# Performance work log

Hardware: AMD Instinct MI355X
Metric: run time of the kernel (lower is better)

The kernel has to match this reference:

```python
import jax, jax.numpy as jnp
import numpy as np

N, C, H, W = 32, 64, 128, 128
P_ROLL_H, P_ROLL_W = 1, -2  # frozen values of random.randint(-2, 2) at init

def setup_inputs() -> dict:
    key = jax.random.key(0)
    k1, k2, k3 = jax.random.split(key, 3)
    x = jax.random.normal(k1, (N, C, H, W), dtype=jnp.float32)
    # Conv2d(c, c, (1,7), dilation=(1,3), padding=(0,9), bias=False); torch default kaiming-uniform-ish, use uniform
    fan_in = C * 1 * 7
    bc = 1.0 / np.sqrt(fan_in)
    W_conv = jax.random.uniform(k2, (C, C, 1, 7), minval=-bc, maxval=bc, dtype=jnp.float32)
    # p_4_w: uniform(-sqrt(3/3), sqrt(3/3)) = uniform(-1, 1), shape (3,1)
    p4w = jax.random.uniform(k3, (3, 1), minval=-1.0, maxval=1.0, dtype=jnp.float32)
    return {"x": x, "W_conv": W_conv, "p4w": p4w}

def _dilated_unfold_h(x):
    # F.unfold(x, (3,1), dilation=(2,1), padding=(2,0)) -> (n, c, 3, h, w)
    # tap k gathers row h + 2*(k-1), zero-padded
    xp = jnp.pad(x, ((0, 0), (0, 0), (2, 2), (0, 0)))
    h = x.shape[2]
    return jnp.stack([xp[:, :, 2 * k:2 * k + h, :] for k in range(3)], axis=2)

def reference(x, W_conv, p4w):
    # t_1: dilated 3-tap unfold along h -> (n, c, 3, h, w)
    t1 = _dilated_unfold_h(x)
    # t_2: circular rolls along h and w
    t2 = jnp.roll(jnp.roll(t1, P_ROLL_H, axis=3), P_ROLL_W, axis=4)
    # t_3: conv (1,7) dilation (1,3) pad (0,9), width-preserving
    t3 = jax.lax.conv_general_dilated(
        x, W_conv, window_strides=(1, 1), padding=((0, 0), (9, 9)),
        rhs_dilation=(1, 3), dimension_numbers=("NCHW", "OIHW", "NCHW"))
    # t_4: weighted reduce over the 3 taps (einsum 'abcde,cf->abfde', f=1)
    t4 = jnp.einsum("nckhw,kf->ncfhw", t2, p4w)[:, :, 0]
    # t_6 = (x + conv(x)) * t_4
    return (x + t3) * t4
```

## Files before the change

### kernel.cpp

```cpp
#include <hip/hip_runtime.h>
#include <hip/hip_bf16.h>

#define N_ 32
#define C_ 64
#define H_ 128
#define W_ 128
#define HW_ (H_ * W_)
#define CHW_ (C_ * HW_)

#define XT_STRIDE 72
#define XT_ROWS 146
#define CB_STRIDE 130
#define SMEM_BYTES (4 * 16 * CB_STRIDE * 4)

typedef __bf16 bf16x8 __attribute__((ext_vector_type(8)));
typedef float floatx4 __attribute__((ext_vector_type(4)));

__device__ inline unsigned short f2bf(float f) {
    __hip_bfloat16 h = __float2bfloat16(f);
    return *reinterpret_cast<unsigned short*>(&h);
}

__global__ void prepack_kernel(const float* __restrict__ Wc, uint4* __restrict__ Ap) {
    int idx = blockIdx.x * 256 + threadIdx.x;
    if (idx >= 14 * 4 * 64) return;
    int lane = idx & 63;
    int mt = (idx >> 6) & 3;
    int kt = idx >> 8;
    int m = mt * 16 + (lane & 15);
    int kbase = kt * 32 + (lane >> 4) * 8;
    unsigned int r[4];
    #pragma unroll
    for (int p = 0; p < 4; ++p) {
        unsigned int half[2];
        #pragma unroll
        for (int jj = 0; jj < 2; ++jj) {
            int k = kbase + 2 * p + jj;
            int t = k >> 6;
            int i = k & 63;
            half[jj] = f2bf(Wc[m * 448 + i * 7 + t]);
        }
        r[p] = half[0] | (half[1] << 16);
    }
    Ap[idx] = make_uint4(r[0], r[1], r[2], r[3]);
}

__global__ __launch_bounds__(256) void fused_mfma_kernel(
    const float* __restrict__ x, const uint4* __restrict__ Ap,
    const float* __restrict__ p4w, float* __restrict__ out)
{
    __shared__ __attribute__((aligned(16))) char smem[SMEM_BYTES];
    unsigned short* xT = (unsigned short*)smem;
    float* convbuf = (float*)smem;

    const int b = blockIdx.x;
    const int xcd = b & 7;
    const int i_ = b >> 3;
    const int n = i_ >> 4;
    const int h = xcd * 16 + (i_ & 15);

    const int tid = threadIdx.x;
    const int wave = tid >> 6;
    const int lane = tid & 63;
    const int l16 = lane & 15;
    const int quad = lane >> 4;
    const float* xn = x + (size_t)n * CHW_;

    uint4 afrag[14];
    #pragma unroll
    for (int kt = 0; kt < 14; ++kt)
        afrag[kt] = Ap[kt * 256 + wave * 64 + lane];

    unsigned int* xz = (unsigned int*)xT;
    for (int i = tid; i < 648; i += 256) {
        int d = (i < 324) ? i : (4932 + (i - 324));
        xz[d] = 0u;
    }

    const float* xrow = xn + h * W_;
    #pragma unroll
    for (int p = 0; p < 4; ++p) {
        const int c0 = wave * 8 + (p >> 1) * 32;
        const int w = (tid & 63) + (p & 1) * 64;
        const float* src = xrow + (size_t)c0 * HW_ + w;
        unsigned int pk[4];
        #pragma unroll
        for (int i = 0; i < 4; ++i) {
            float f0 = src[(size_t)(2 * i) * HW_];
            float f1 = src[(size_t)(2 * i + 1) * HW_];
            pk[i] = (unsigned int)f2bf(f0) | ((unsigned int)f2bf(f1) << 16);
        }
        *(uint4*)&xT[(w + 9) * XT_STRIDE + c0] = make_uint4(pk[0], pk[1], pk[2], pk[3]);
    }

    __syncthreads();

    floatx4 acc[8];
    #pragma unroll
    for (int nt = 0; nt < 8; ++nt) acc[nt] = (floatx4){0.f, 0.f, 0.f, 0.f};

    const int base_half = l16 * XT_STRIDE + quad * 8;
    #pragma unroll
    for (int kt = 0; kt < 14; ++kt) {
        bf16x8 av = __builtin_bit_cast(bf16x8, afrag[kt]);
        int koff = (kt >> 1) * 3 * XT_STRIDE + (kt & 1) * 32;
        #pragma unroll
        for (int nt = 0; nt < 8; ++nt) {
            int off = base_half + koff + nt * 16 * XT_STRIDE;
            uint4 d = *(const uint4*)&xT[off];
            bf16x8 bv = __builtin_bit_cast(bf16x8, d);
            acc[nt] = __builtin_amdgcn_mfma_f32_16x16x32_bf16(av, bv, acc[nt], 0, 0, 0);
        }
    }

    __syncthreads();

    float* cw = convbuf + wave * 16 * CB_STRIDE;
    #pragma unroll
    for (int nt = 0; nt < 8; ++nt) {
        #pragma unroll
        for (int r = 0; r < 4; ++r)
            cw[(quad * 4 + r) * CB_STRIDE + nt * 16 + l16] = acc[nt][r];
    }

    const float p0 = p4w[0], p1 = p4w[1], p2 = p4w[2];
    const int h1 = (h - 1 + H_) & 127;

    #pragma unroll
    for (int j = 0; j < 8; ++j) {
        int idx = j * 64 + lane;
        int o_ = idx >> 5;
        int w4 = idx & 31;
        int w = w4 * 4;
        int o = wave * 16 + o_;

        float4 cv = *(const float4*)&cw[o_ * CB_STRIDE + w];

        const float* xc = xn + o * HW_;
        float4 xv = *(const float4*)(xc + h * W_ + w);

        int wsrc = w + 2;
        float tap[3][4];
        #pragma unroll
        for (int k = 0; k < 3; ++k) {
            int hh = h1 + 2 * k - 2;
            if (hh >= 0 && hh < H_) {
                const float* rowp = xc + hh * W_;
                float2 a = *(const float2*)(rowp + wsrc);
                float2 b2 = *(const float2*)(rowp + ((wsrc + 2) & 127));
                tap[k][0] = a.x; tap[k][1] = a.y; tap[k][2] = b2.x; tap[k][3] = b2.y;
            } else {
                tap[k][0] = tap[k][1] = tap[k][2] = tap[k][3] = 0.f;
            }
        }
        float ov[4];
        float xa[4] = {xv.x, xv.y, xv.z, xv.w};
        float ca[4] = {cv.x, cv.y, cv.z, cv.w};
        #pragma unroll
        for (int e = 0; e < 4; ++e) {
            float t4 = p0 * tap[0][e] + p1 * tap[1][e] + p2 * tap[2][e];
            ov[e] = (xa[e] + ca[e]) * t4;
        }
        *(float4*)(out + (size_t)n * CHW_ + o * HW_ + h * W_ + w) =
            make_float4(ov[0], ov[1], ov[2], ov[3]);
    }
}

extern "C" void kernel_launch(void* const* d_in, const int* in_sizes, int n_in,
                              void* d_out, int out_size, void* d_ws, size_t ws_size,
                              hipStream_t stream) {
    const float* x   = (const float*)d_in[0];
    const float* Wc  = (const float*)d_in[1];
    const float* p4w = (const float*)d_in[2];
    float* out       = (float*)d_out;
    uint4* Apack     = (uint4*)d_ws;

    prepack_kernel<<<14, 256, 0, stream>>>(Wc, Apack);
    fused_mfma_kernel<<<N_ * H_, 256, 0, stream>>>(x, Apack, p4w, out);
}
```

Measured before the change: 265.3 us.

## Cut LDS and register footprint to raise occupancy of fused conv kernel

The staging buffer for the conv result is halved: the epilogue now writes and consumes results in two width halves, and shared memory shrinks to the size of the transposed input tile. The 14 preloaded weight fragments are replaced by a one-ahead streamed load of each fragment inside the MFMA loop, which frees VGPRs. A launch-bounds occupancy hint of 6 is added. The aim is more resident blocks per CU to hide global-memory latency. The cost is weight loads now sitting on the MFMA critical path and possible register spills under the tighter bound.

```diff
diff --git a/kernel.cpp b/kernel.cpp
--- a/kernel.cpp
+++ b/kernel.cpp
@@ -10,8 +10,8 @@
 
 #define XT_STRIDE 72
 #define XT_ROWS 146
-#define CB_STRIDE 130
-#define SMEM_BYTES (4 * 16 * CB_STRIDE * 4)
+#define CB_STRIDE 68
+#define SMEM_BYTES (XT_ROWS * XT_STRIDE * 2)
 
 typedef __bf16 bf16x8 __attribute__((ext_vector_type(8)));
 typedef float floatx4 __attribute__((ext_vector_type(4)));
@@ -45,7 +45,7 @@
     Ap[idx] = make_uint4(r[0], r[1], r[2], r[3]);
 }
 
-__global__ __launch_bounds__(256) void fused_mfma_kernel(
+__global__ __launch_bounds__(256, 6) void fused_mfma_kernel(
     const float* __restrict__ x, const uint4* __restrict__ Ap,
     const float* __restrict__ p4w, float* __restrict__ out)
 {
@@ -66,10 +66,8 @@
     const int quad = lane >> 4;
     const float* xn = x + (size_t)n * CHW_;
 
-    uint4 afrag[14];
-    #pragma unroll
-    for (int kt = 0; kt < 14; ++kt)
-        afrag[kt] = Ap[kt * 256 + wave * 64 + lane];
+    const uint4* ApW = Ap + wave * 64 + lane;
+    uint4 bcur = ApW[0];
 
     unsigned int* xz = (unsigned int*)xT;
     for (int i = tid; i < 648; i += 256) {
@@ -102,7 +100,8 @@
     const int base_half = l16 * XT_STRIDE + quad * 8;
     #pragma unroll
     for (int kt = 0; kt < 14; ++kt) {
-        bf16x8 av = __builtin_bit_cast(bf16x8, afrag[kt]);
+        uint4 bnext = ApW[((kt < 13) ? (kt + 1) : 13) * 256];
+        bf16x8 av = __builtin_bit_cast(bf16x8, bcur);
         int koff = (kt >> 1) * 3 * XT_STRIDE + (kt & 1) * 32;
         #pragma unroll
         for (int nt = 0; nt < 8; ++nt) {
@@ -111,58 +110,60 @@
             bf16x8 bv = __builtin_bit_cast(bf16x8, d);
             acc[nt] = __builtin_amdgcn_mfma_f32_16x16x32_bf16(av, bv, acc[nt], 0, 0, 0);
         }
+        bcur = bnext;
     }
 
     __syncthreads();
 
-    float* cw = convbuf + wave * 16 * CB_STRIDE;
-    #pragma unroll
-    for (int nt = 0; nt < 8; ++nt) {
-        #pragma unroll
-        for (int r = 0; r < 4; ++r)
-            cw[(quad * 4 + r) * CB_STRIDE + nt * 16 + l16] = acc[nt][r];
-    }
-
     const float p0 = p4w[0], p1 = p4w[1], p2 = p4w[2];
     const int h1 = (h - 1 + H_) & 127;
+    float* cw = convbuf + wave * 16 * CB_STRIDE;
 
     #pragma unroll
-    for (int j = 0; j < 8; ++j) {
-        int idx = j * 64 + lane;
-        int o_ = idx >> 5;
-        int w4 = idx & 31;
-        int w = w4 * 4;
-        int o = wave * 16 + o_;
+    for (int hb = 0; hb < 2; ++hb) {
+        #pragma unroll
+        for (int nt = 0; nt < 4; ++nt) {
+            #pragma unroll
+            for (int r = 0; r < 4; ++r)
+                cw[(quad * 4 + r) * CB_STRIDE + nt * 16 + l16] = acc[hb * 4 + nt][r];
+        }
+        #pragma unroll
+        for (int j2 = 0; j2 < 4; ++j2) {
+            int o_ = j2 * 4 + quad;
+            int w = hb * 64 + l16 * 4;
+            int o = wave * 16 + o_;
 
-        float4 cv = *(const float4*)&cw[o_ * CB_STRIDE + w];
+            float4 cv = *(const float4*)&cw[o_ * CB_STRIDE + l16 * 4];
 
-        const float* xc = xn + o * HW_;
-        float4 xv = *(const float4*)(xc + h * W_ + w);
+            const float* xc = xn + o * HW_;
+            float4 xv = *(const float4*)(xc + h * W_ + w);
 
-        int wsrc = w + 2;
-        float tap[3][4];
-        #pragma unroll
-        for (int k = 0; k < 3; ++k) {
-            int hh = h1 + 2 * k - 2;
-            if (hh >= 0 && hh < H_) {
-                const float* rowp = xc + hh * W_;
-                float2 a = *(const float2*)(rowp + wsrc);
-                float2 b2 = *(const float2*)(rowp + ((wsrc + 2) & 127));
-                tap[k][0] = a.x; tap[k][1] = a.y; tap[k][2] = b2.x; tap[k][3] = b2.y;
-            } else {
-                tap[k][0] = tap[k][1] = tap[k][2] = tap[k][3] = 0.f;
+            int wsa = w + 2;
+            int wsb = (w + 4) & 127;
+            float tap[3][4];
+            #pragma unroll
+            for (int k = 0; k < 3; ++k) {
+                int hh = h1 + 2 * k - 2;
+                if (hh >= 0 && hh < H_) {
+                    const float* rowp = xc + hh * W_;
+                    float2 a = *(const float2*)(rowp + wsa);
+                    float2 b2 = *(const float2*)(rowp + wsb);
+                    tap[k][0] = a.x; tap[k][1] = a.y; tap[k][2] = b2.x; tap[k][3] = b2.y;
+                } else {
+                    tap[k][0] = tap[k][1] = tap[k][2] = tap[k][3] = 0.f;
+                }
             }
+            float ov[4];
+            float xa[4] = {xv.x, xv.y, xv.z, xv.w};
+            float ca[4] = {cv.x, cv.y, cv.z, cv.w};
+            #pragma unroll
+            for (int e = 0; e < 4; ++e) {
+                float t4 = p0 * tap[0][e] + p1 * tap[1][e] + p2 * tap[2][e];
+                ov[e] = (xa[e] + ca[e]) * t4;
+            }
+            *(float4*)(out + (size_t)n * CHW_ + o * HW_ + h * W_ + w) =
+                make_float4(ov[0], ov[1], ov[2], ov[3]);
         }
-        float ov[4];
-        float xa[4] = {xv.x, xv.y, xv.z, xv.w};
-        float ca[4] = {cv.x, cv.y, cv.z, cv.w};
-        #pragma unroll
-        for (int e = 0; e < 4; ++e) {
-            float t4 = p0 * tap[0][e] + p1 * tap[1][e] + p2 * tap[2][e];
-            ov[e] = (xa[e] + ca[e]) * t4;
-        }
-        *(float4*)(out + (size_t)n * CHW_ + o * HW_ + h * W_ + w) =
-            make_float4(ov[0], ov[1], ov[2], ov[3]);
     }
 }
 
```

Result: slower. 281.6 us (+6.1%).

## Split MFMA work by width columns per wave and stream weight fragments

Applied to the files above, without the earlier changes.

Each wave now computes all 64 output channels for a 32-column slice of the row, instead of 16 channels across all 128 columns. This cuts LDS B-fragment reads per wave, since two B tiles are reused across four A tiles. The 14 preloaded A fragments in registers are replaced by loads of the next k-step's four A fragments from global/L2 inside the loop. The conv result must now be exchanged across waves through LDS, which adds an extra __syncthreads and puts weight fetches on the critical loop path.

```diff
diff --git a/kernel.cpp b/kernel.cpp
--- a/kernel.cpp
+++ b/kernel.cpp
@@ -11,7 +11,7 @@
 #define XT_STRIDE 72
 #define XT_ROWS 146
 #define CB_STRIDE 130
-#define SMEM_BYTES (4 * 16 * CB_STRIDE * 4)
+#define SMEM_BYTES (64 * CB_STRIDE * 4)
 
 typedef __bf16 bf16x8 __attribute__((ext_vector_type(8)));
 typedef float floatx4 __attribute__((ext_vector_type(4)));
@@ -66,10 +66,7 @@
     const int quad = lane >> 4;
     const float* xn = x + (size_t)n * CHW_;
 
-    uint4 afrag[14];
-    #pragma unroll
-    for (int kt = 0; kt < 14; ++kt)
-        afrag[kt] = Ap[kt * 256 + wave * 64 + lane];
+    const uint4* Apl = Ap + lane;
 
     unsigned int* xz = (unsigned int*)xT;
     for (int i = tid; i < 648; i += 256) {
@@ -93,38 +90,62 @@
         *(uint4*)&xT[(w + 9) * XT_STRIDE + c0] = make_uint4(pk[0], pk[1], pk[2], pk[3]);
     }
 
+    uint4 a0 = Apl[0 * 64];
+    uint4 a1 = Apl[1 * 64];
+    uint4 a2 = Apl[2 * 64];
+    uint4 a3 = Apl[3 * 64];
+
     __syncthreads();
 
     floatx4 acc[8];
     #pragma unroll
-    for (int nt = 0; nt < 8; ++nt) acc[nt] = (floatx4){0.f, 0.f, 0.f, 0.f};
-
-    const int base_half = l16 * XT_STRIDE + quad * 8;
+    for (int i = 0; i < 8; ++i) acc[i] = (floatx4){0.f, 0.f, 0.f, 0.f};
+
+    const int base_half = (wave * 2) * 16 * XT_STRIDE + l16 * XT_STRIDE + quad * 8;
     #pragma unroll
     for (int kt = 0; kt < 14; ++kt) {
-        bf16x8 av = __builtin_bit_cast(bf16x8, afrag[kt]);
-        int koff = (kt >> 1) * 3 * XT_STRIDE + (kt & 1) * 32;
-        #pragma unroll
-        for (int nt = 0; nt < 8; ++nt) {
-            int off = base_half + koff + nt * 16 * XT_STRIDE;
-            uint4 d = *(const uint4*)&xT[off];
-            bf16x8 bv = __builtin_bit_cast(bf16x8, d);
-            acc[nt] = __builtin_amdgcn_mfma_f32_16x16x32_bf16(av, bv, acc[nt], 0, 0, 0);
-        }
+        const int ktn = (kt < 13) ? (kt + 1) : 13;
+        uint4 n0 = Apl[ktn * 256 + 0 * 64];
+        uint4 n1 = Apl[ktn * 256 + 1 * 64];
+        uint4 n2 = Apl[ktn * 256 + 2 * 64];
+        uint4 n3 = Apl[ktn * 256 + 3 * 64];
+
+        const int koff = (kt >> 1) * 3 * XT_STRIDE + (kt & 1) * 32;
+        uint4 d0 = *(const uint4*)&xT[base_half + koff];
+        uint4 d1 = *(const uint4*)&xT[base_half + koff + 16 * XT_STRIDE];
+        bf16x8 b0 = __builtin_bit_cast(bf16x8, d0);
+        bf16x8 b1 = __builtin_bit_cast(bf16x8, d1);
+
+        acc[0] = __builtin_amdgcn_mfma_f32_16x16x32_bf16(__builtin_bit_cast(bf16x8, a0), b0, acc[0], 0, 0, 0);
+        acc[1] = __builtin_amdgcn_mfma_f32_16x16x32_bf16(__builtin_bit_cast(bf16x8, a0), b1, acc[1], 0, 0, 0);
+        acc[2] = __builtin_amdgcn_mfma_f32_16x16x32_bf16(__builtin_bit_cast(bf16x8, a1), b0, acc[2], 0, 0, 0);
+        acc[3] = __builtin_amdgcn_mfma_f32_16x16x32_bf16(__builtin_bit_cast(bf16x8, a1), b1, acc[3], 0, 0, 0);
+        acc[4] = __builtin_amdgcn_mfma_f32_16x16x32_bf16(__builtin_bit_cast(bf16x8, a2), b0, acc[4], 0, 0, 0);
+        acc[5] = __builtin_amdgcn_mfma_f32_16x16x32_bf16(__builtin_bit_cast(bf16x8, a2), b1, acc[5], 0, 0, 0);
+        acc[6] = __builtin_amdgcn_mfma_f32_16x16x32_bf16(__builtin_bit_cast(bf16x8, a3), b0, acc[6], 0, 0, 0);
+        acc[7] = __builtin_amdgcn_mfma_f32_16x16x32_bf16(__builtin_bit_cast(bf16x8, a3), b1, acc[7], 0, 0, 0);
+
+        a0 = n0; a1 = n1; a2 = n2; a3 = n3;
     }
 
     __syncthreads();
 
-    float* cw = convbuf + wave * 16 * CB_STRIDE;
-    #pragma unroll
-    for (int nt = 0; nt < 8; ++nt) {
-        #pragma unroll
-        for (int r = 0; r < 4; ++r)
-            cw[(quad * 4 + r) * CB_STRIDE + nt * 16 + l16] = acc[nt][r];
-    }
+    #pragma unroll
+    for (int ot = 0; ot < 4; ++ot) {
+        #pragma unroll
+        for (int j = 0; j < 2; ++j) {
+            #pragma unroll
+            for (int r = 0; r < 4; ++r)
+                convbuf[(ot * 16 + quad * 4 + r) * CB_STRIDE + wave * 32 + j * 16 + l16] =
+                    acc[ot * 2 + j][r];
+        }
+    }
+
+    __syncthreads();
 
     const float p0 = p4w[0], p1 = p4w[1], p2 = p4w[2];
     const int h1 = (h - 1 + H_) & 127;
+    const float* cw = convbuf + wave * 16 * CB_STRIDE;
 
     #pragma unroll
     for (int j = 0; j < 8; ++j) {
```

Measured after the change: 273.5 us. +3.1%, slower.
